# Kernel tuning notes

Hardware: AMD Instinct MI355X
Metric: run time of the kernel (lower is better)

Reference implementation:

```python
import jax, jax.numpy as jnp
import numpy as np

NUM_CLASSES = 43
IMG_SIZE = 640.0
ALPHA, GAMMA = 0.25, 2.0
EPS = 1e-07


def _focal_loss(pred, target):
    p = jnp.clip(pred, EPS, 1.0 - EPS)
    pos = (target > 0.5).astype(p.dtype)
    neg = (target <= 0.5).astype(p.dtype)
    pos_loss = -ALPHA * (1.0 - p) ** GAMMA * jnp.log(p) * pos * target
    neg_loss = -(1.0 - ALPHA) * p ** GAMMA * jnp.log(1.0 - p) * neg * (1.0 - target)
    num_pos = jnp.maximum(pos.sum(), 1.0)
    return (pos_loss + neg_loss).sum() / num_pos


def _generate_targets(bboxes, labels, h, w):
    # bboxes: [B, M, 4] x1y1x2y2 in pixels; labels: [B, M] int (-1 = pad)
    B, M = labels.shape
    stride = IMG_SIZE / h
    x1, y1, x2, y2 = [bboxes[..., i] for i in range(4)]
    cx, cy = (x1 + x2) / 2.0, (y1 + y2) / 2.0
    bw, bh = x2 - x1, y2 - y1
    valid = (labels >= 0) & (bboxes.sum(-1) > 0) & (bw > 0) & (bh > 0)  # [B, M]

    gx = jnp.clip((cx / stride).astype(jnp.int32), 0, w - 1)
    gy = jnp.clip((cy / stride).astype(jnp.int32), 0, h - 1)
    # radius = sqrt(bw*bh)/stride clamped to >=2, then truncated to int
    r = jnp.maximum(jnp.sqrt(bw * bh) / stride, 2.0).astype(jnp.int32).astype(jnp.float32)
    sigma = r / 2.0

    gxf = gx.astype(jnp.float32)[:, :, None, None]  # [B,M,1,1]
    gyf = gy.astype(jnp.float32)[:, :, None, None]
    xg = jnp.arange(w, dtype=jnp.float32)[None, None, None, :]
    yg = jnp.arange(h, dtype=jnp.float32)[None, None, :, None]
    dist_sq = (xg - gxf) ** 2 + (yg - gyf) ** 2  # [B,M,H,W]
    r4 = r[:, :, None, None]
    s4 = sigma[:, :, None, None]
    gauss = jnp.exp(-dist_sq / (2.0 * s4 * s4))
    gauss = gauss * (dist_sq <= (2.0 * r4) ** 2) * valid[:, :, None, None]
    heatmap = gauss.max(axis=1)[:, None]  # [B,1,H,W]; max with implicit 0 init (gauss>=0)

    grid_cx = (gx.astype(jnp.float32) + 0.5) * stride
    grid_cy = (gy.astype(jnp.float32) + 0.5) * stride
    dx = (cx - grid_cx) / stride
    dy = (cy - grid_cy) / stride
    dw = jnp.log(bw / stride + 1e-06)
    dh = jnp.log(bh / stride + 1e-06)

    b_idx = jnp.broadcast_to(jnp.arange(B)[:, None], (B, M))
    gy_s = jnp.where(valid, gy, h)  # out-of-bounds -> dropped
    lab_s = jnp.clip(labels, 0, NUM_CLASSES - 1)

    box_targets = jnp.zeros((B, 4, h, w), jnp.float32)
    box_targets = box_targets.at[b_idx, 0, gy_s, gx].set(dx, mode='drop')
    box_targets = box_targets.at[b_idx, 1, gy_s, gx].set(dy, mode='drop')
    box_targets = box_targets.at[b_idx, 2, gy_s, gx].set(dw, mode='drop')
    box_targets = box_targets.at[b_idx, 3, gy_s, gx].set(dh, mode='drop')
    class_targets = jnp.zeros((B, NUM_CLASSES, h, w), jnp.float32)
    class_targets = class_targets.at[b_idx, lab_s, gy_s, gx].set(1.0, mode='drop')
    mask = jnp.zeros((B, 1, h, w), jnp.float32)
    mask = mask.at[b_idx, 0, gy_s, gx].set(1.0, mode='drop')
    return heatmap, box_targets, class_targets, mask


def setup_inputs() -> dict:
    key = jax.random.key(0)
    k1, k2, k3, k4, k5, k6 = jax.random.split(key, 6)
    B, M, H, W = 16, 64, 160, 160
    pred_heatmap = jax.random.uniform(k1, (B, 1, H, W), jnp.float32)
    pred_boxes = jax.random.normal(k2, (B, 4, H, W), jnp.float32)
    pred_classes = jax.random.normal(k3, (B, NUM_CLASSES, H, W), jnp.float32)
    pts = jax.random.uniform(k4, (B, M, 2, 2), jnp.float32) * IMG_SIZE  # two corners
    lo = jnp.min(pts, axis=2)
    hi = jnp.max(pts, axis=2) + 1.0
    bboxes = jnp.concatenate([lo, hi], axis=-1)  # x1,y1,x2,y2
    labels = jax.random.randint(k5, (B, M), 0, NUM_CLASSES)
    drop = jax.random.uniform(k6, (B, M)) < 0.3
    labels = jnp.where(drop, -1, labels).astype(jnp.int64)
    return {"pred_heatmap": pred_heatmap, "pred_boxes": pred_boxes,
            "pred_classes": pred_classes, "bboxes": bboxes, "labels": labels}


def reference(pred_heatmap, pred_boxes, pred_classes, bboxes, labels):
    B, _, h, w = pred_heatmap.shape
    t_heat, t_box, t_cls, mask = _generate_targets(bboxes, labels, h, w)
    heat_loss = _focal_loss(pred_heatmap, t_heat)
    num_pos = jnp.maximum(mask.sum(), 1.0)
    l1 = jnp.abs(pred_boxes * mask - t_box * mask).sum()
    box_loss = jnp.where(num_pos > 1, l1 / num_pos, 0.0)
    cmask = jnp.broadcast_to(mask, t_cls.shape)
    cls_raw = _focal_loss(jax.nn.sigmoid(pred_classes) * cmask, t_cls * cmask)
    cls_loss = jnp.where(num_pos > 1, cls_raw, 0.0)
    total = heat_loss + box_loss + cls_loss  # lambdas all 1.0
    return total
```

## Files before the change

### kernel.cpp

```cpp
#include <hip/hip_runtime.h>

#define HH 160
#define WW 160
#define HW (HH*WW)
#define NB 16
#define NM 64
#define NC 43
#define BLKX 25
#define NHEAT (NB*BLKX)
#define NCELL (NB*16)

constexpr float STRIDE = 4.0f;
constexpr float EPSF = 1e-7f;
constexpr float BIGF = 3.4e38f;

__device__ __forceinline__ void box_geom4(const float4* __restrict__ bb4,
                                          const int* __restrict__ labels, int t,
                                          bool& valid, int& gx, int& gy,
                                          float& cx, float& cy, float& bw, float& bh) {
  float4 v = bb4[t];
  cx = (v.x + v.z) * 0.5f;
  cy = (v.y + v.w) * 0.5f;
  bw = v.z - v.x;
  bh = v.w - v.y;
  int lab = labels[t];
  valid = (lab >= 0) && ((v.x + v.y + v.z + v.w) > 0.0f) && (bw > 0.0f) && (bh > 0.0f);
  int tgx = (int)(cx * 0.25f);
  int tgy = (int)(cy * 0.25f);
  gx = tgx < 0 ? 0 : (tgx > WW - 1 ? WW - 1 : tgx);
  gy = tgy < 0 ? 0 : (tgy > HH - 1 ? HH - 1 : tgy);
}

__global__ __launch_bounds__(256) void k_fused(const float* __restrict__ pred_heat,
                                               const float* __restrict__ pred_boxes,
                                               const float* __restrict__ pred_classes,
                                               const float4* __restrict__ bboxes,
                                               const int* __restrict__ labels,
                                               float2* __restrict__ heatp,
                                               float4* __restrict__ cellsp) {
  __shared__ float4 sp[NM];
  __shared__ float lred[4];
  __shared__ int nred[4];
  __shared__ float4 cred[4];

  int b = blockIdx.y, bx = blockIdx.x;
  int tid = threadIdx.x;
  int wave = tid >> 6, lane = tid & 63;

  if (tid < NM) {
    int t = b * NM + tid;
    bool valid; int gx, gy; float cx, cy, bw, bh;
    box_geom4(bboxes, labels, t, valid, gx, gy, cx, cy, bw, bh);
    float rf = fmaxf(sqrtf(bw * bh) * 0.25f, 2.0f);
    float r = (float)(int)rf;
    float z = 2.0f / (r * r);
    float gxf = (float)gx, gyf = (float)gy;
    float4 p;
    p.x = z;
    p.y = -2.0f * z * gxf;
    p.z = -2.0f * z * gyf;
    p.w = valid ? z * fmaf(gxf, gxf, gyf * gyf) : __int_as_float(0x7fc00000);
    sp[tid] = p;
  }
  __syncthreads();

  int pixbase = bx * 1024 + tid * 4;
  int idx = b * HW + pixbase;
  float4 pr4 = *(const float4*)(pred_heat + idx);
  int row = pixbase / WW;
  float xf0 = (float)(pixbase - row * WW);
  float yf = (float)row;
  float xf1 = xf0 + 1.0f, xf2 = xf0 + 2.0f, xf3 = xf0 + 3.0f;
  float yy = yf * yf;
  float s0 = fmaf(xf0, xf0, yy), s1 = fmaf(xf1, xf1, yy);
  float s2 = fmaf(xf2, xf2, yy), s3 = fmaf(xf3, xf3, yy);

  float m0 = BIGF, m1 = BIGF, m2 = BIGF, m3 = BIGF;
  #pragma unroll
  for (int m = 0; m < NM; m += 2) {
    float4 c0 = sp[m], c1 = sp[m + 1];
    { float base = fmaf(c0.z, yf, c0.w);
      m0 = fminf(m0, fmaf(c0.x, s0, fmaf(c0.y, xf0, base)));
      m1 = fminf(m1, fmaf(c0.x, s1, fmaf(c0.y, xf1, base)));
      m2 = fminf(m2, fmaf(c0.x, s2, fmaf(c0.y, xf2, base)));
      m3 = fminf(m3, fmaf(c0.x, s3, fmaf(c0.y, xf3, base))); }
    { float base = fmaf(c1.z, yf, c1.w);
      m0 = fminf(m0, fmaf(c1.x, s0, fmaf(c1.y, xf0, base)));
      m1 = fminf(m1, fmaf(c1.x, s1, fmaf(c1.y, xf1, base)));
      m2 = fminf(m2, fmaf(c1.x, s2, fmaf(c1.y, xf2, base)));
      m3 = fminf(m3, fmaf(c1.x, s3, fmaf(c1.y, xf3, base))); }
  }

  float t0 = (m0 <= 8.0f) ? __expf(-m0) : 0.0f;
  float t1 = (m1 <= 8.0f) ? __expf(-m1) : 0.0f;
  float t2 = (m2 <= 8.0f) ? __expf(-m2) : 0.0f;
  float t3 = (m3 <= 8.0f) ? __expf(-m3) : 0.0f;
  float p0 = fminf(fmaxf(pr4.x, EPSF), 1.0f - EPSF);
  float p1 = fminf(fmaxf(pr4.y, EPSF), 1.0f - EPSF);
  float p2 = fminf(fmaxf(pr4.z, EPSF), 1.0f - EPSF);
  float p3 = fminf(fmaxf(pr4.w, EPSF), 1.0f - EPSF);
  float q0 = 1.0f - p0, q1 = 1.0f - p1, q2 = 1.0f - p2, q3 = 1.0f - p3;
  bool o0 = t0 > 0.5f, o1 = t1 > 0.5f, o2 = t2 > 0.5f, o3 = t3 > 0.5f;
  float lg0 = __logf(o0 ? p0 : q0), lg1 = __logf(o1 ? p1 : q1);
  float lg2 = __logf(o2 ? p2 : q2), lg3 = __logf(o3 ? p3 : q3);
  float cf0 = o0 ? (-0.25f * q0 * q0 * t0) : (-0.75f * p0 * p0 * (1.0f - t0));
  float cf1 = o1 ? (-0.25f * q1 * q1 * t1) : (-0.75f * p1 * p1 * (1.0f - t1));
  float cf2 = o2 ? (-0.25f * q2 * q2 * t2) : (-0.75f * p2 * p2 * (1.0f - t2));
  float cf3 = o3 ? (-0.25f * q3 * q3 * t3) : (-0.75f * p3 * p3 * (1.0f - t3));
  float loss = fmaf(cf0, lg0, cf1 * lg1) + fmaf(cf2, lg2, cf3 * lg3);

  int cnt = __popcll(__ballot(o0)) + __popcll(__ballot(o1)) +
            __popcll(__ballot(o2)) + __popcll(__ballot(o3));
  #pragma unroll
  for (int off = 32; off > 0; off >>= 1) loss += __shfl_down(loss, off);
  if (lane == 0) { lred[wave] = loss; nred[wave] = cnt; }
  __syncthreads();
  if (tid == 0)
    heatp[b * BLKX + bx] = make_float2(lred[0] + lred[1] + lred[2] + lred[3],
                                       (float)(nred[0] + nred[1] + nred[2] + nred[3]));

  if (bx < 16) {
    int m = bx * 4 + wave;
    int lbox = b * NM + lane;
    bool valid; int gx, gy; float cx, cy, bw, bh;
    box_geom4(bboxes, labels, lbox, valid, gx, gy, cx, cy, bw, bh);
    int lab = labels[lbox]; lab = lab < 0 ? 0 : (lab > NC - 1 ? NC - 1 : lab);

    int   valid_m = __shfl((int)valid, m);
    int   gx_m = __shfl(gx, m), gy_m = __shfl(gy, m);
    float cx_m = __shfl(cx, m), cy_m = __shfl(cy, m);
    float bw_m = __shfl(bw, m), bh_m = __shfl(bh, m);

    float l1 = 0.0f, csum = 0.0f;
    float cnt1 = 0.0f, npos = 0.0f;
    if (valid_m) {
      bool maps = valid && (gx == gx_m) && (gy == gy_m);
      unsigned long long mk = __ballot(maps);
      if ((63 - __clzll(mk)) == m) {
        unsigned long long cm = maps ? (1ull << lab) : 0ull;
        #pragma unroll
        for (int o = 1; o < 64; o <<= 1) cm |= __shfl_xor(cm, o);
        int celloff = gy_m * WW + gx_m;
        if (lane < NC) {
          float x = pred_classes[(size_t)b * NC * HW + (size_t)lane * HW + celloff];
          float s = 1.0f / (1.0f + __expf(-x));
          float pc = fminf(fmaxf(s, EPSF), 1.0f - EPSF);
          float omc = 1.0f - pc;
          csum = ((cm >> lane) & 1ull) ? (-0.25f * omc * omc * __logf(pc))
                                       : (-0.75f * pc * pc * __logf(omc));
        }
        #pragma unroll
        for (int o = 32; o > 0; o >>= 1) csum += __shfl_down(csum, o);
        if (lane == 0) {
          float dxv = (cx_m - ((float)gx_m + 0.5f) * STRIDE) * 0.25f;
          float dyv = (cy_m - ((float)gy_m + 0.5f) * STRIDE) * 0.25f;
          float dwv = __logf(bw_m * 0.25f + 1e-6f);
          float dhv = __logf(bh_m * 0.25f + 1e-6f);
          const float* pb = pred_boxes + (size_t)b * 4 * HW + celloff;
          l1 = fabsf(pb[0] - dxv) + fabsf(pb[HW] - dyv) +
               fabsf(pb[2 * HW] - dwv) + fabsf(pb[3 * HW] - dhv);
          cnt1 = 1.0f;
          npos = (float)__popcll(cm);
        }
      }
    }
    if (lane == 0) cred[wave] = make_float4(l1, cnt1, csum, npos);
    __syncthreads();
    if (tid == 0) {
      float4 a = cred[0], c1 = cred[1], c2 = cred[2], c3 = cred[3];
      cellsp[b * 16 + bx] = make_float4(a.x + c1.x + c2.x + c3.x,
                                        a.y + c1.y + c2.y + c3.y,
                                        a.z + c1.z + c2.z + c3.z,
                                        a.w + c1.w + c2.w + c3.w);
    }
  }
}

__global__ __launch_bounds__(256) void k_final(const float2* __restrict__ heatp,
                                               const float4* __restrict__ cellsp,
                                               float* __restrict__ out) {
  int t = threadIdx.x;
  double hs = 0.0, hc = 0.0, l1 = 0.0, mc = 0.0, cs = 0.0, cp = 0.0;
  for (int i = t; i < NHEAT; i += 256) {
    float2 v = heatp[i];
    hs += (double)v.x; hc += (double)v.y;
  }
  if (t < NCELL) {
    float4 e = cellsp[t];
    l1 = (double)e.x; mc = (double)e.y; cs = (double)e.z; cp = (double)e.w;
  }
  #pragma unroll
  for (int off = 32; off > 0; off >>= 1) {
    hs += __shfl_down(hs, off); hc += __shfl_down(hc, off);
    l1 += __shfl_down(l1, off); mc += __shfl_down(mc, off);
    cs += __shfl_down(cs, off); cp += __shfl_down(cp, off);
  }
  __shared__ double fin[4][6];
  int wave = t >> 6;
  if ((t & 63) == 0) {
    fin[wave][0] = hs; fin[wave][1] = hc; fin[wave][2] = l1;
    fin[wave][3] = mc; fin[wave][4] = cs; fin[wave][5] = cp;
  }
  __syncthreads();
  if (t == 0) {
    double HS = 0, HC = 0, L1 = 0, MC = 0, CS = 0, CP = 0;
    #pragma unroll
    for (int i = 0; i < 4; ++i) {
      HS += fin[i][0]; HC += fin[i][1]; L1 += fin[i][2];
      MC += fin[i][3]; CS += fin[i][4]; CP += fin[i][5];
    }
    double nph = HC < 1.0 ? 1.0 : HC;
    float heat = (float)(HS / nph);
    float box = 0.0f, cls = 0.0f;
    if (MC > 1.5) {
      box = (float)(L1 / MC);
      double c = CP < 1.0 ? 1.0 : CP;
      cls = (float)(CS / c);
    }
    out[0] = heat + box + cls;
  }
}

extern "C" void kernel_launch(void* const* d_in, const int* in_sizes, int n_in,
                              void* d_out, int out_size, void* d_ws, size_t ws_size,
                              hipStream_t stream) {
  const float*  pred_heat    = (const float*)d_in[0];
  const float*  pred_boxes   = (const float*)d_in[1];
  const float*  pred_classes = (const float*)d_in[2];
  const float4* bboxes       = (const float4*)d_in[3];
  const int*    labels       = (const int*)d_in[4];

  char* ws = (char*)d_ws;
  float2* heatp  = (float2*)ws;
  float4* cellsp = (float4*)(ws + 3200);

  dim3 grid(BLKX, NB);
  k_fused<<<grid, 256, 0, stream>>>(pred_heat, pred_boxes, pred_classes,
                                    bboxes, labels, heatp, cellsp);
  k_final<<<1, 256, 0, stream>>>(heatp, cellsp, (float*)d_out);
}
```

Measured before the change: 13.68 us.

## Hoist cell gathers ahead of heatmap loop and widen final reduction block

Moves the pred_heat load and the scattered pred_classes/pred_boxes gathers for winning cells to the start of the kernel, so their latency overlaps the shared-memory setup and the gaussian min loop. The box L1 terms are now loaded in parallel by lanes 43-46 and reduced with the class sum, instead of four serial loads on lane 0. The final kernel uses 512 threads so each heat partial is read once without a loop. Keeping the gathered values live across the heavy loop adds register pressure.

Result: slower. 14.45 us (+5.6%).

```diff
diff --git a/kernel.cpp b/kernel.cpp
--- a/kernel.cpp
+++ b/kernel.cpp
@@ -47,6 +47,45 @@
   int tid = threadIdx.x;
   int wave = tid >> 6, lane = tid & 63;
 
+  int pixbase = bx * 1024 + tid * 4;
+  int idx = b * HW + pixbase;
+  float4 pr4 = *(const float4*)(pred_heat + idx);
+
+  bool cellsblk = (bx < 16);
+  bool iswin = false;
+  float xcls = 0.0f, pbv = 0.0f;
+  unsigned long long cm = 0;
+  float cx_m, cy_m, bw_m, bh_m;
+  int gx_m, gy_m;
+  if (cellsblk) {
+    int m = bx * 4 + wave;
+    int lbox = b * NM + lane;
+    bool valid; int gx, gy; float cx, cy, bw, bh;
+    box_geom4(bboxes, labels, lbox, valid, gx, gy, cx, cy, bw, bh);
+    int lab = labels[lbox]; lab = lab < 0 ? 0 : (lab > NC - 1 ? NC - 1 : lab);
+
+    int valid_m = __shfl((int)valid, m);
+    gx_m = __shfl(gx, m); gy_m = __shfl(gy, m);
+    cx_m = __shfl(cx, m); cy_m = __shfl(cy, m);
+    bw_m = __shfl(bw, m); bh_m = __shfl(bh, m);
+
+    if (valid_m) {
+      bool maps = valid && (gx == gx_m) && (gy == gy_m);
+      unsigned long long mk = __ballot(maps);
+      if ((63 - __clzll(mk)) == m) {
+        iswin = true;
+        cm = maps ? (1ull << lab) : 0ull;
+        #pragma unroll
+        for (int o = 1; o < 64; o <<= 1) cm |= __shfl_xor(cm, o);
+        int celloff = gy_m * WW + gx_m;
+        if (lane < NC)
+          xcls = pred_classes[(size_t)b * NC * HW + (size_t)lane * HW + celloff];
+        else if (lane < NC + 4)
+          pbv = pred_boxes[(size_t)b * 4 * HW + (size_t)(lane - NC) * HW + celloff];
+      }
+    }
+  }
+
   if (tid < NM) {
     int t = b * NM + tid;
     bool valid; int gx, gy; float cx, cy, bw, bh;
@@ -64,9 +103,6 @@
   }
   __syncthreads();
 
-  int pixbase = bx * 1024 + tid * 4;
-  int idx = b * HW + pixbase;
-  float4 pr4 = *(const float4*)(pred_heat + idx);
   int row = pixbase / WW;
   float xf0 = (float)(pixbase - row * WW);
   float yf = (float)row;
@@ -119,50 +155,31 @@
     heatp[b * BLKX + bx] = make_float2(lred[0] + lred[1] + lred[2] + lred[3],
                                        (float)(nred[0] + nred[1] + nred[2] + nred[3]));
 
-  if (bx < 16) {
-    int m = bx * 4 + wave;
-    int lbox = b * NM + lane;
-    bool valid; int gx, gy; float cx, cy, bw, bh;
-    box_geom4(bboxes, labels, lbox, valid, gx, gy, cx, cy, bw, bh);
-    int lab = labels[lbox]; lab = lab < 0 ? 0 : (lab > NC - 1 ? NC - 1 : lab);
-
-    int   valid_m = __shfl((int)valid, m);
-    int   gx_m = __shfl(gx, m), gy_m = __shfl(gy, m);
-    float cx_m = __shfl(cx, m), cy_m = __shfl(cy, m);
-    float bw_m = __shfl(bw, m), bh_m = __shfl(bh, m);
-
-    float l1 = 0.0f, csum = 0.0f;
-    float cnt1 = 0.0f, npos = 0.0f;
-    if (valid_m) {
-      bool maps = valid && (gx == gx_m) && (gy == gy_m);
-      unsigned long long mk = __ballot(maps);
-      if ((63 - __clzll(mk)) == m) {
-        unsigned long long cm = maps ? (1ull << lab) : 0ull;
-        #pragma unroll
-        for (int o = 1; o < 64; o <<= 1) cm |= __shfl_xor(cm, o);
-        int celloff = gy_m * WW + gx_m;
-        if (lane < NC) {
-          float x = pred_classes[(size_t)b * NC * HW + (size_t)lane * HW + celloff];
-          float s = 1.0f / (1.0f + __expf(-x));
-          float pc = fminf(fmaxf(s, EPSF), 1.0f - EPSF);
-          float omc = 1.0f - pc;
-          csum = ((cm >> lane) & 1ull) ? (-0.25f * omc * omc * __logf(pc))
-                                       : (-0.75f * pc * pc * __logf(omc));
-        }
-        #pragma unroll
-        for (int o = 32; o > 0; o >>= 1) csum += __shfl_down(csum, o);
-        if (lane == 0) {
-          float dxv = (cx_m - ((float)gx_m + 0.5f) * STRIDE) * 0.25f;
-          float dyv = (cy_m - ((float)gy_m + 0.5f) * STRIDE) * 0.25f;
-          float dwv = __logf(bw_m * 0.25f + 1e-6f);
-          float dhv = __logf(bh_m * 0.25f + 1e-6f);
-          const float* pb = pred_boxes + (size_t)b * 4 * HW + celloff;
-          l1 = fabsf(pb[0] - dxv) + fabsf(pb[HW] - dyv) +
-               fabsf(pb[2 * HW] - dwv) + fabsf(pb[3 * HW] - dhv);
-          cnt1 = 1.0f;
-          npos = (float)__popcll(cm);
-        }
+  if (cellsblk) {
+    float l1 = 0.0f, csum = 0.0f, cnt1 = 0.0f, npos = 0.0f;
+    if (iswin) {
+      if (lane < NC) {
+        float s = 1.0f / (1.0f + __expf(-xcls));
+        float pc = fminf(fmaxf(s, EPSF), 1.0f - EPSF);
+        float omc = 1.0f - pc;
+        csum = ((cm >> lane) & 1ull) ? (-0.25f * omc * omc * __logf(pc))
+                                     : (-0.75f * pc * pc * __logf(omc));
       }
+      float dxv = (cx_m - ((float)gx_m + 0.5f) * STRIDE) * 0.25f;
+      float dyv = (cy_m - ((float)gy_m + 0.5f) * STRIDE) * 0.25f;
+      int li = lane - NC;
+      float tlin = (li == 0) ? dxv : dyv;
+      float tlog = __logf(((li == 2) ? bw_m : bh_m) * 0.25f + 1e-6f);
+      float targ = (li < 2) ? tlin : tlog;
+      float l1c = (li >= 0 && li < 4) ? fabsf(pbv - targ) : 0.0f;
+      #pragma unroll
+      for (int o = 32; o > 0; o >>= 1) {
+        csum += __shfl_down(csum, o);
+        l1c  += __shfl_down(l1c, o);
+      }
+      l1 = l1c;
+      cnt1 = (lane == 0) ? 1.0f : 0.0f;
+      npos = (float)__popcll(cm);
     }
     if (lane == 0) cred[wave] = make_float4(l1, cnt1, csum, npos);
     __syncthreads();
@@ -176,14 +193,14 @@
   }
 }
 
-__global__ __launch_bounds__(256) void k_final(const float2* __restrict__ heatp,
+__global__ __launch_bounds__(512) void k_final(const float2* __restrict__ heatp,
                                                const float4* __restrict__ cellsp,
                                                float* __restrict__ out) {
   int t = threadIdx.x;
   double hs = 0.0, hc = 0.0, l1 = 0.0, mc = 0.0, cs = 0.0, cp = 0.0;
-  for (int i = t; i < NHEAT; i += 256) {
-    float2 v = heatp[i];
-    hs += (double)v.x; hc += (double)v.y;
+  if (t < NHEAT) {
+    float2 v = heatp[t];
+    hs = (double)v.x; hc = (double)v.y;
   }
   if (t < NCELL) {
     float4 e = cellsp[t];
@@ -195,7 +212,7 @@
     l1 += __shfl_down(l1, off); mc += __shfl_down(mc, off);
     cs += __shfl_down(cs, off); cp += __shfl_down(cp, off);
   }
-  __shared__ double fin[4][6];
+  __shared__ double fin[8][6];
   int wave = t >> 6;
   if ((t & 63) == 0) {
     fin[wave][0] = hs; fin[wave][1] = hc; fin[wave][2] = l1;
@@ -205,7 +222,7 @@
   if (t == 0) {
     double HS = 0, HC = 0, L1 = 0, MC = 0, CS = 0, CP = 0;
     #pragma unroll
-    for (int i = 0; i < 4; ++i) {
+    for (int i = 0; i < 8; ++i) {
       HS += fin[i][0]; HC += fin[i][1]; L1 += fin[i][2];
       MC += fin[i][3]; CS += fin[i][4]; CP += fin[i][5];
     }
@@ -237,5 +254,5 @@
   dim3 grid(BLKX, NB);
   k_fused<<<grid, 256, 0, stream>>>(pred_heat, pred_boxes, pred_classes,
                                     bboxes, labels, heatp, cellsp);
-  k_final<<<1, 256, 0, stream>>>(heatp, cellsp, (float*)d_out);
-}
+  k_final<<<1, 512, 0, stream>>>(heatp, cellsp, (float*)d_out);
+}
```
